# Kernel tuning notes

Hardware: AMD Instinct MI355X
Metric: run time of the kernel (lower is better)

The kernel has to match this reference:

```python
import jax, jax.numpy as jnp
import numpy as np

N_NODES = 100000
HIDDEN = 128
N_EDGES = 1000000


def setup_inputs() -> dict:
    key = jax.random.key(0)
    k1, k2, k3 = jax.random.split(key, 3)
    z = jax.random.normal(k1, (N_NODES, HIDDEN), dtype=jnp.float32)
    edge_index = jax.random.randint(k2, (2, N_EDGES), 0, N_NODES, dtype=jnp.int64)
    # xavier_uniform for square matrix: bound = sqrt(6/(fan_in+fan_out))
    bound = float(np.sqrt(6.0 / (HIDDEN + HIDDEN)))
    weights = jax.random.uniform(k3, (HIDDEN, HIDDEN), dtype=jnp.float32,
                                 minval=-bound, maxval=bound)
    return {"z": z, "edge_index": edge_index, "weights": weights}


def reference(z, edge_index, weights):
    # symm=True: symmetrize the bilinear form
    W = weights + weights.T                      # [d, d]
    z_src = z[edge_index[0]]                     # [E, d] gather
    z_dst = z[edge_index[1]]                     # [E, d] gather
    # torch: (W @ z_dst.T).T == z_dst @ W.T
    value = jnp.einsum('ed,dk,ek->e', z_src, W, z_dst)  # row-wise bilinear score
    return jax.nn.sigmoid(value)
```

## Files before the change

kernel.cpp:

```cpp
#include <hip/hip_runtime.h>

#define HIDDEN 128
#define SLOT_H 264

typedef _Float16 f16;
typedef f16 f16x2 __attribute__((ext_vector_type(2)));
typedef f16 f16x8 __attribute__((ext_vector_type(8)));
typedef float f32x16 __attribute__((ext_vector_type(16)));

static __device__ __forceinline__ float fdot2(f16x2 a, f16x2 b, float c) {
    return __builtin_amdgcn_fdot2(a, b, c, false);
}

__global__ __launch_bounds__(256) void prep_w(const float* __restrict__ w,
                                              f16* __restrict__ wsh_t) {
    int idx = blockIdx.x * 256 + threadIdx.x;
    int n = idx >> 7, k = idx & 127;
    wsh_t[idx] = (f16)(w[k * HIDDEN + n] + w[n * HIDDEN + k]);
}

__global__ __launch_bounds__(256, 3) void gemm_mfma2(const float* __restrict__ z,
                                                     const f16* __restrict__ wsh_t,
                                                     f16* __restrict__ zh,
                                                     f16* __restrict__ uh, int nrows) {
    __shared__ f16 afrag[64 * SLOT_H];
    int tid = threadIdx.x;
    int row0 = blockIdx.x * 128;
    if (row0 > nrows - 128) row0 = nrows - 128;

    {
        const float4* zg = (const float4*)(z + (size_t)row0 * HIDDEN);
        f16x8* zhg = (f16x8*)(zh + (size_t)row0 * HIDDEN);
        #pragma unroll
        for (int it = 0; it < 8; ++it) {
            int g = it * 256 + tid;
            float4 v0 = zg[2 * g];
            float4 v1 = zg[2 * g + 1];
            f16x8 h = {(f16)v0.x, (f16)v0.y, (f16)v0.z, (f16)v0.w,
                       (f16)v1.x, (f16)v1.y, (f16)v1.z, (f16)v1.w};
            zhg[g] = h;
            int row = g >> 4, ch = g & 15;
            int slot = (row >> 5) * 16 + ch;
            *(f16x8*)&afrag[slot * SLOT_H + (row & 31) * 8] = h;
        }
    }
    __syncthreads();

    int wave = tid >> 6, lane = tid & 63;
    int m = lane & 31, half = lane >> 5;

    const f16* wb = wsh_t + (size_t)m * HIDDEN + half * 8;

    f32x16 acc0, acc1, acc2, acc3;
    #pragma unroll
    for (int r = 0; r < 16; ++r) { acc0[r] = 0.f; acc1[r] = 0.f; acc2[r] = 0.f; acc3[r] = 0.f; }

    #pragma unroll
    for (int ks = 0; ks < 8; ++ks) {
        f16x8 a = *(const f16x8*)&afrag[(wave * 16 + ks * 2 + half) * SLOT_H + m * 8];
        f16x8 b0 = *(const f16x8*)&wb[ 0 * HIDDEN + 16 * ks];
        f16x8 b1 = *(const f16x8*)&wb[32 * HIDDEN + 16 * ks];
        f16x8 b2 = *(const f16x8*)&wb[64 * HIDDEN + 16 * ks];
        f16x8 b3 = *(const f16x8*)&wb[96 * HIDDEN + 16 * ks];
        acc0 = __builtin_amdgcn_mfma_f32_32x32x16_f16(a, b0, acc0, 0, 0, 0);
        acc1 = __builtin_amdgcn_mfma_f32_32x32x16_f16(a, b1, acc1, 0, 0, 0);
        acc2 = __builtin_amdgcn_mfma_f32_32x32x16_f16(a, b2, acc2, 0, 0, 0);
        acc3 = __builtin_amdgcn_mfma_f32_32x32x16_f16(a, b3, acc3, 0, 0, 0);
    }

    f16* ur = uh + (size_t)(row0 + wave * 32) * HIDDEN;
    #pragma unroll
    for (int r = 0; r < 16; ++r) {
        int row = (r & 3) + 8 * (r >> 2) + 4 * half;
        f16* p = ur + (size_t)row * HIDDEN + m;
        p[0]  = (f16)acc0[r];
        p[32] = (f16)acc1[r];
        p[64] = (f16)acc2[r];
        p[96] = (f16)acc3[r];
    }
}

__global__ __launch_bounds__(256) void edge_score16(const f16* __restrict__ uh,
                                                    const f16* __restrict__ zh,
                                                    const int* __restrict__ eidx,
                                                    float* __restrict__ out, int E) {
    int tid = threadIdx.x;
    int g = tid >> 4, t = tid & 15;
    int e = blockIdx.x * 16 + g;
    if (e >= E) return;
    int src = eidx[e];
    int dst = eidx[E + e];
    const float4* a4 = (const float4*)(uh + (size_t)src * HIDDEN);
    const float4* b4 = (const float4*)(zh + (size_t)dst * HIDDEN);
    float4 av = a4[t], bv = b4[t];
    const f16x2* ap = (const f16x2*)&av;
    const f16x2* bp = (const f16x2*)&bv;
    float s = 0.f;
    #pragma unroll
    for (int i = 0; i < 4; ++i) s = fdot2(ap[i], bp[i], s);
    #pragma unroll
    for (int off = 8; off > 0; off >>= 1) s += __shfl_down(s, off, 16);
    if (t == 0) out[e] = 1.0f / (1.0f + __expf(-s));
}

extern "C" void kernel_launch(void* const* d_in, const int* in_sizes, int n_in,
                              void* d_out, int out_size, void* d_ws, size_t ws_size,
                              hipStream_t stream) {
    const float* z    = (const float*)d_in[0];
    const int*   eidx = (const int*)d_in[1];
    const float* w    = (const float*)d_in[2];
    float* out = (float*)d_out;

    int nrows = in_sizes[0] / HIDDEN;
    int E = out_size;

    f16* wsh_t = (f16*)d_ws;
    f16* zh    = wsh_t + HIDDEN * HIDDEN;
    f16* uh    = zh + (size_t)nrows * HIDDEN;

    prep_w<<<(HIDDEN * HIDDEN) / 256, 256, 0, stream>>>(w, wsh_t);
    gemm_mfma2<<<(nrows + 127) / 128, 256, 0, stream>>>(z, wsh_t, zh, uh, nrows);
    edge_score16<<<(E + 15) / 16, 256, 0, stream>>>(uh, zh, eidx, out, E);
}
```

Measured before the change: 177.3 us.

## Bin edges by destination node and remap blocks across XCDs for locality

Adds a counting-sort pass (histogram, scan, scatter) that groups edges into buckets of 1024 destination nodes. Each edge is packed with its source, destination and original id into one 64-bit word. The edge kernel then walks the sorted list, and block ids are remapped so each of the 8 XCDs gets a contiguous range, aiming for better L2 reuse of zh rows. In exchange it adds three extra kernel launches, a single-thread serial scan, global atomics, and an 8 MB permutation buffer. The output is now written in scattered order, and the path falls back to the old kernel if the workspace is too small.

Measured after the change: 193.6 us. +9.2%, slower.

```diff
diff --git a/kernel.cpp b/kernel.cpp
--- a/kernel.cpp
+++ b/kernel.cpp
@@ -2,21 +2,78 @@
 
 #define HIDDEN 128
 #define SLOT_H 264
+#define BSHIFT 10
+#define NBMAX 128
 
 typedef _Float16 f16;
 typedef f16 f16x2 __attribute__((ext_vector_type(2)));
 typedef f16 f16x8 __attribute__((ext_vector_type(8)));
 typedef float f32x16 __attribute__((ext_vector_type(16)));
+typedef unsigned long long ull;
 
 static __device__ __forceinline__ float fdot2(f16x2 a, f16x2 b, float c) {
     return __builtin_amdgcn_fdot2(a, b, c, false);
 }
 
 __global__ __launch_bounds__(256) void prep_w(const float* __restrict__ w,
-                                              f16* __restrict__ wsh_t) {
+                                              f16* __restrict__ wsh_t,
+                                              int* __restrict__ hist) {
     int idx = blockIdx.x * 256 + threadIdx.x;
+    if (idx < 2 * NBMAX) hist[idx] = 0;
     int n = idx >> 7, k = idx & 127;
     wsh_t[idx] = (f16)(w[k * HIDDEN + n] + w[n * HIDDEN + k]);
+}
+
+__global__ __launch_bounds__(256) void hist_k(const int* __restrict__ eidx,
+                                              int* __restrict__ hist, int E, int nb) {
+    __shared__ int h[NBMAX];
+    int tid = threadIdx.x;
+    if (tid < NBMAX) h[tid] = 0;
+    __syncthreads();
+    for (int e = blockIdx.x * 256 + tid; e < E; e += gridDim.x * 256)
+        atomicAdd(&h[eidx[E + e] >> BSHIFT], 1);
+    __syncthreads();
+    if (tid < nb && h[tid]) atomicAdd(&hist[tid], h[tid]);
+}
+
+__global__ void scan_k(const int* __restrict__ hist, int* __restrict__ cursor, int nb) {
+    if (threadIdx.x == 0) {
+        int s = 0;
+        for (int i = 0; i < nb; ++i) { cursor[i] = s; s += hist[i]; }
+    }
+}
+
+__global__ __launch_bounds__(256) void scatter_k(const int* __restrict__ eidx,
+                                                 int* __restrict__ cursor,
+                                                 ull* __restrict__ perm, int E, int nb) {
+    __shared__ int lh[NBMAX], lbase[NBMAX], lrank[NBMAX];
+    int tid = threadIdx.x;
+    int base = blockIdx.x * 4096;
+    if (tid < NBMAX) { lh[tid] = 0; lrank[tid] = 0; }
+    __syncthreads();
+    int s[16], d[16], bb[16];
+    #pragma unroll
+    for (int i = 0; i < 16; ++i) {
+        int e = base + i * 256 + tid;
+        bb[i] = -1;
+        if (e < E) {
+            s[i] = eidx[e]; d[i] = eidx[E + e];
+            bb[i] = d[i] >> BSHIFT;
+            atomicAdd(&lh[bb[i]], 1);
+        }
+    }
+    __syncthreads();
+    if (tid < nb && lh[tid]) lbase[tid] = atomicAdd(&cursor[tid], lh[tid]);
+    __syncthreads();
+    #pragma unroll
+    for (int i = 0; i < 16; ++i) {
+        if (bb[i] >= 0) {
+            int e = base + i * 256 + tid;
+            int r = atomicAdd(&lrank[bb[i]], 1);
+            perm[lbase[bb[i]] + r] =
+                (ull)s[i] | ((ull)d[i] << 17) | ((ull)e << 34);
+        }
+    }
 }
 
 __global__ __launch_bounds__(256, 3) void gemm_mfma2(const float* __restrict__ z,
@@ -48,7 +105,6 @@
 
     int wave = tid >> 6, lane = tid & 63;
     int m = lane & 31, half = lane >> 5;
-
     const f16* wb = wsh_t + (size_t)m * HIDDEN + half * 8;
 
     f32x16 acc0, acc1, acc2, acc3;
@@ -78,6 +134,33 @@
         p[64] = (f16)acc2[r];
         p[96] = (f16)acc3[r];
     }
+}
+
+__global__ __launch_bounds__(256) void edge_bin(const f16* __restrict__ uh,
+                                                const f16* __restrict__ zh,
+                                                const ull* __restrict__ perm,
+                                                float* __restrict__ out, int E, int cpx) {
+    int tid = threadIdx.x;
+    int g = tid >> 4, t = tid & 15;
+    int b = blockIdx.x;
+    int chunk = (b & 7) * cpx + (b >> 3);
+    int e = chunk * 16 + g;
+    if (e >= E) return;
+    ull p = perm[e];
+    int src = (int)(p & 0x1FFFF);
+    int dst = (int)((p >> 17) & 0x1FFFF);
+    int eid = (int)(p >> 34);
+    const float4* a4 = (const float4*)(uh + (size_t)src * HIDDEN);
+    const float4* b4 = (const float4*)(zh + (size_t)dst * HIDDEN);
+    float4 av = a4[t], bv = b4[t];
+    const f16x2* ap = (const f16x2*)&av;
+    const f16x2* bp = (const f16x2*)&bv;
+    float s = 0.f;
+    #pragma unroll
+    for (int i = 0; i < 4; ++i) s = fdot2(ap[i], bp[i], s);
+    #pragma unroll
+    for (int off = 8; off > 0; off >>= 1) s += __shfl_down(s, off, 16);
+    if (t == 0) out[eid] = 1.0f / (1.0f + __expf(-s));
 }
 
 __global__ __launch_bounds__(256) void edge_score16(const f16* __restrict__ uh,
@@ -113,12 +196,30 @@
 
     int nrows = in_sizes[0] / HIDDEN;
     int E = out_size;
+    int nb = (nrows >> BSHIFT) + 1;
 
     f16* wsh_t = (f16*)d_ws;
     f16* zh    = wsh_t + HIDDEN * HIDDEN;
     f16* uh    = zh + (size_t)nrows * HIDDEN;
-
-    prep_w<<<(HIDDEN * HIDDEN) / 256, 256, 0, stream>>>(w, wsh_t);
+    int* hist  = (int*)(uh + (size_t)nrows * HIDDEN);
+    int* cursor = hist + NBMAX;
+    ull* perm  = (ull*)(cursor + NBMAX);
+
+    size_t need = (size_t)((char*)(perm + E) - (char*)d_ws);
+    bool binned = ws_size >= need;
+
+    prep_w<<<64, 256, 0, stream>>>(w, wsh_t, hist);
+    if (binned) {
+        hist_k<<<256, 256, 0, stream>>>(eidx, hist, E, nb);
+        scan_k<<<1, 64, 0, stream>>>(hist, cursor, nb);
+        scatter_k<<<(E + 4095) / 4096, 256, 0, stream>>>(eidx, cursor, perm, E, nb);
+    }
     gemm_mfma2<<<(nrows + 127) / 128, 256, 0, stream>>>(z, wsh_t, zh, uh, nrows);
-    edge_score16<<<(E + 15) / 16, 256, 0, stream>>>(uh, zh, eidx, out, E);
-}
+    if (binned) {
+        int nch = (E + 15) / 16;
+        int cpx = (nch + 7) / 8;
+        edge_bin<<<8 * cpx, 256, 0, stream>>>(uh, zh, perm, out, E, cpx);
+    } else {
+        edge_score16<<<(E + 15) / 16, 256, 0, stream>>>(uh, zh, eidx, out, E);
+    }
+}
```
